# Optimization experiments

Measured on AMD Instinct MI355X. Metric: run time of the kernel, lower is better.

The kernel has to match this reference:

```python
import jax, jax.numpy as jnp
import numpy as np

N_NODES = 8192
DIM = 512

def setup_inputs() -> dict:
    key = jax.random.key(0)
    k1, k2, k3, k4 = jax.random.split(key, 4)
    x = jax.random.normal(k1, (N_NODES, DIM), dtype=jnp.float32)
    adj = jax.random.uniform(k2, (N_NODES, N_NODES), dtype=jnp.float32)
    # nn.Linear(dim, dim): weight [out, in], bias [out]
    bound = 1.0 / np.sqrt(DIM)
    W = jax.random.uniform(k3, (DIM, DIM), minval=-bound, maxval=bound, dtype=jnp.float32)
    b = jax.random.uniform(k4, (DIM,), minval=-bound, maxval=bound, dtype=jnp.float32)
    return {"x": x, "adj": adj, "W": W, "b": b}

def reference(x, adj, W, b):
    # agg = adj @ x : [N, dim]
    agg = jnp.matmul(adj, x)
    # Linear: agg @ W.T + b, then ReLU
    out = jnp.matmul(agg, W.T) + b
    return jax.nn.relu(out)
```

## Files before the change

kernel.cpp:

```cpp
#include <hip/hip_runtime.h>
#include <stdint.h>

typedef __bf16 bf16_t;
typedef bf16_t bf16x8 __attribute__((ext_vector_type(8)));
typedef float f32x4 __attribute__((ext_vector_type(4)));

#define N_NODES 8192
#define DIM 512

typedef __attribute__((address_space(1))) void as1_void;
typedef __attribute__((address_space(3))) void as3_void;

__device__ __forceinline__ void gload_lds16(const void* g, void* l) {
  __builtin_amdgcn_global_load_lds((as1_void*)g, (as3_void*)l, 16, 0, 0);
}

__global__ __launch_bounds__(256) void k_yw(const float* __restrict__ x,
                                            const float* __restrict__ W,
                                            bf16_t* __restrict__ Yt) {
  constexpr int NIT = DIM / 32;
  __shared__ float As[2][128 * 32];
  __shared__ float Bs[2][128 * 32];

  const int b = blockIdx.x;
  const int n0 = (b & 3) * 128;
  const int k0 = (b >> 2) * 128;

  const int t = threadIdx.x;
  const int lane = t & 63;
  const int w = t >> 6;
  const int wr = w & 1;
  const int wc = w >> 1;
  const int lrow = lane & 15;
  const int quad = lane >> 4;

  const int srow = t >> 3;
  const int aoff = ((t & 7) ^ (srow & 7)) * 4;
  const float* ag = W + (size_t)(n0 + srow) * DIM + aoff;
  const float* bg = x + (size_t)(k0 + srow) * DIM + aoff;

  auto stage = [&](int it, int buf) {
    const int kc = it * 32;
#pragma unroll
    for (int i = 0; i < 4; ++i) {
      gload_lds16(ag + (size_t)(i * 32) * DIM + kc, &As[buf][(i * 256 + t) * 4]);
      gload_lds16(bg + (size_t)(i * 32) * DIM + kc, &Bs[buf][(i * 256 + t) * 4]);
    }
  };

  const int apc0 = ((quad * 2) ^ (lrow & 7)) * 4;
  const int apc1 = (((quad * 2) ^ (lrow & 7)) ^ 1) * 4;

  f32x4 acc[4][4] = {};

  auto compute = [&](int buf) {
    bf16x8 af[4], bfr[4];
#pragma unroll
    for (int ii = 0; ii < 4; ++ii) {
      const int rb = (wr * 64 + ii * 16 + lrow) * 32;
      f32x4 a0 = *(const f32x4*)&As[buf][rb + apc0];
      f32x4 a1 = *(const f32x4*)&As[buf][rb + apc1];
#pragma unroll
      for (int z = 0; z < 4; ++z) {
        af[ii][z] = (bf16_t)a0[z];
        af[ii][z + 4] = (bf16_t)a1[z];
      }
    }
#pragma unroll
    for (int jj = 0; jj < 4; ++jj) {
      const int rb = (wc * 64 + jj * 16 + lrow) * 32;
      f32x4 b0 = *(const f32x4*)&Bs[buf][rb + apc0];
      f32x4 b1 = *(const f32x4*)&Bs[buf][rb + apc1];
#pragma unroll
      for (int z = 0; z < 4; ++z) {
        bfr[jj][z] = (bf16_t)b0[z];
        bfr[jj][z + 4] = (bf16_t)b1[z];
      }
    }
#pragma unroll
    for (int ii = 0; ii < 4; ++ii)
#pragma unroll
      for (int jj = 0; jj < 4; ++jj)
        acc[ii][jj] =
            __builtin_amdgcn_mfma_f32_16x16x32_bf16(af[ii], bfr[jj], acc[ii][jj], 0, 0, 0);
  };

  stage(0, 0);
  __syncthreads();
  int cur = 0;
#pragma unroll 1
  for (int it = 0; it < NIT; ++it) {
    if (it + 1 < NIT) stage(it + 1, cur ^ 1);
    compute(cur);
    __syncthreads();
    cur ^= 1;
  }

#pragma unroll
  for (int ii = 0; ii < 4; ++ii)
#pragma unroll
    for (int jj = 0; jj < 4; ++jj) {
      const int col = k0 + wc * 64 + jj * 16 + lrow;
#pragma unroll
      for (int r = 0; r < 4; ++r) {
        const int row = n0 + wr * 64 + ii * 16 + quad * 4 + r;
        Yt[(size_t)row * N_NODES + col] = (bf16_t)acc[ii][jj][r];
      }
    }
}

__global__ __launch_bounds__(256) void k_main(const float* __restrict__ A,
                                              const bf16_t* __restrict__ Bt,
                                              const float* __restrict__ bias,
                                              float* __restrict__ out) {
  constexpr int K = N_NODES;
  constexpr int NIT = K / 32;
  __shared__ float As[4][64 * 32];
  __shared__ bf16_t Bs[4][128 * 32];

  const int b = blockIdx.x;
  const int xcd = b & 7;
  const int i6 = b >> 3;
  const int n_tile = i6 & 3;
  const int mg = i6 >> 2;
  const int m0 = (mg * 8 + xcd) * 64;
  const int n0 = n_tile * 128;

  const int t = threadIdx.x;
  const int lane = t & 63;
  const int w = t >> 6;
  const int wr = w & 1;
  const int wc = w >> 1;
  const int lrow = lane & 15;
  const int quad = lane >> 4;

  const int aoff = ((t & 7) ^ ((t >> 3) & 7)) * 4;
  const int boff = ((t & 3) ^ ((t >> 3) & 3)) * 8;
  const float* ag = A + (size_t)(m0 + (t >> 3)) * K + aoff;
  const bf16_t* bg = Bt + (size_t)(n0 + (t >> 2)) * K + boff;

  auto stage = [&](int it, int buf) {
    const int kc = it * 32;
#pragma unroll
    for (int i = 0; i < 2; ++i)
      gload_lds16(ag + (size_t)(i * 32) * K + kc, &As[buf][(i * 256 + t) * 4]);
#pragma unroll
    for (int i = 0; i < 2; ++i)
      gload_lds16(bg + (size_t)(i * 64) * K + kc, &Bs[buf][(i * 256 + t) * 8]);
  };

  const int apc0 = ((quad * 2) ^ (lrow & 7)) * 4;
  const int apc1 = (((quad * 2) ^ (lrow & 7)) ^ 1) * 4;
  const int bpc = (quad ^ ((lrow >> 1) & 3)) * 8;

  f32x4 acc[2][4] = {};

  auto compute = [&](int buf) {
    bf16x8 af[2], bfr[4];
#pragma unroll
    for (int ii = 0; ii < 2; ++ii) {
      const int rb = (wr * 32 + ii * 16 + lrow) * 32;
      f32x4 a0 = *(const f32x4*)&As[buf][rb + apc0];
      f32x4 a1 = *(const f32x4*)&As[buf][rb + apc1];
#pragma unroll
      for (int z = 0; z < 4; ++z) {
        af[ii][z] = (bf16_t)a0[z];
        af[ii][z + 4] = (bf16_t)a1[z];
      }
    }
#pragma unroll
    for (int jj = 0; jj < 4; ++jj)
      bfr[jj] = *(const bf16x8*)&Bs[buf][(wc * 64 + jj * 16 + lrow) * 32 + bpc];
#pragma unroll
    for (int ii = 0; ii < 2; ++ii)
#pragma unroll
      for (int jj = 0; jj < 4; ++jj)
        acc[ii][jj] =
            __builtin_amdgcn_mfma_f32_16x16x32_bf16(af[ii], bfr[jj], acc[ii][jj], 0, 0, 0);
  };

  float bjv[4];
#pragma unroll
  for (int jj = 0; jj < 4; ++jj) bjv[jj] = bias[n0 + wc * 64 + jj * 16 + lrow];

  stage(0, 0);
  stage(1, 1);
  stage(2, 2);

#pragma unroll 1
  for (int it = 0; it < NIT; ++it) {
    if (it < NIT - 2) {
      asm volatile("s_waitcnt vmcnt(8)" ::: "memory");
    } else if (it == NIT - 2) {
      asm volatile("s_waitcnt vmcnt(4)" ::: "memory");
    } else {
      asm volatile("s_waitcnt vmcnt(0)" ::: "memory");
    }
    asm volatile("s_waitcnt lgkmcnt(0)" ::: "memory");
    asm volatile("s_barrier" ::: "memory");
    if (it + 3 < NIT) stage(it + 3, (it + 3) & 3);
    compute(it & 3);
  }

#pragma unroll
  for (int ii = 0; ii < 2; ++ii)
#pragma unroll
    for (int jj = 0; jj < 4; ++jj) {
      const int col = n0 + wc * 64 + jj * 16 + lrow;
#pragma unroll
      for (int r = 0; r < 4; ++r) {
        const int row = m0 + wr * 32 + ii * 16 + quad * 4 + r;
        float v = acc[ii][jj][r] + bjv[jj];
        out[(size_t)row * DIM + col] = v > 0.0f ? v : 0.0f;
      }
    }
}

extern "C" void kernel_launch(void* const* d_in, const int* in_sizes, int n_in,
                              void* d_out, int out_size, void* d_ws, size_t ws_size,
                              hipStream_t stream) {
  const float* x = (const float*)d_in[0];
  const float* adj = (const float*)d_in[1];
  const float* W = (const float*)d_in[2];
  const float* b = (const float*)d_in[3];
  float* out = (float*)d_out;

  bf16_t* Yt = (bf16_t*)d_ws;

  k_yw<<<dim3(256), 256, 0, stream>>>(x, W, Yt);
  k_main<<<dim3(512), 256, 0, stream>>>(adj, Yt, b, out);
}
```

Measured before the change: 581.0 us.

## Enlarge main GEMM tile to 128x128 and stream B from global into registers

Result: no change. 577.9 us (-0.5%).

```diff
diff --git a/kernel.cpp b/kernel.cpp
--- a/kernel.cpp
+++ b/kernel.cpp
@@ -115,16 +115,11 @@
                                               float* __restrict__ out) {
   constexpr int K = N_NODES;
   constexpr int NIT = K / 32;
-  __shared__ float As[4][64 * 32];
-  __shared__ bf16_t Bs[4][128 * 32];
+  __shared__ float As[4][128 * 32];
 
   const int b = blockIdx.x;
-  const int xcd = b & 7;
-  const int i6 = b >> 3;
-  const int n_tile = i6 & 3;
-  const int mg = i6 >> 2;
-  const int m0 = (mg * 8 + xcd) * 64;
-  const int n0 = n_tile * 128;
+  const int m0 = (((b >> 3) << 1) | (b & 1)) * 128;
+  const int n0 = ((b >> 1) & 3) * 128;
 
   const int t = threadIdx.x;
   const int lane = t & 63;
@@ -135,31 +130,37 @@
   const int quad = lane >> 4;
 
   const int aoff = ((t & 7) ^ ((t >> 3) & 7)) * 4;
-  const int boff = ((t & 3) ^ ((t >> 3) & 3)) * 8;
   const float* ag = A + (size_t)(m0 + (t >> 3)) * K + aoff;
-  const bf16_t* bg = Bt + (size_t)(n0 + (t >> 2)) * K + boff;
 
   auto stage = [&](int it, int buf) {
     const int kc = it * 32;
 #pragma unroll
-    for (int i = 0; i < 2; ++i)
+    for (int i = 0; i < 4; ++i)
       gload_lds16(ag + (size_t)(i * 32) * K + kc, &As[buf][(i * 256 + t) * 4]);
-#pragma unroll
-    for (int i = 0; i < 2; ++i)
-      gload_lds16(bg + (size_t)(i * 64) * K + kc, &Bs[buf][(i * 256 + t) * 8]);
   };
 
   const int apc0 = ((quad * 2) ^ (lrow & 7)) * 4;
   const int apc1 = (((quad * 2) ^ (lrow & 7)) ^ 1) * 4;
-  const int bpc = (quad ^ ((lrow >> 1) & 3)) * 8;
-
-  f32x4 acc[2][4] = {};
-
-  auto compute = [&](int buf) {
-    bf16x8 af[2], bfr[4];
-#pragma unroll
-    for (int ii = 0; ii < 2; ++ii) {
-      const int rb = (wr * 32 + ii * 16 + lrow) * 32;
+
+  const bf16_t* bsrc[4];
+#pragma unroll
+  for (int jj = 0; jj < 4; ++jj)
+    bsrc[jj] = Bt + (size_t)(n0 + wc * 64 + jj * 16 + lrow) * K + quad * 8;
+
+  bf16x8 bA[4], bB[4];
+  auto loadB = [&](int it, bf16x8* dst) {
+    const int kc = it * 32;
+#pragma unroll
+    for (int jj = 0; jj < 4; ++jj) dst[jj] = *(const bf16x8*)(bsrc[jj] + kc);
+  };
+
+  f32x4 acc[4][4] = {};
+
+  auto compute = [&](int buf, const bf16x8* bfr) {
+    bf16x8 af[4];
+#pragma unroll
+    for (int ii = 0; ii < 4; ++ii) {
+      const int rb = (wr * 64 + ii * 16 + lrow) * 32;
       f32x4 a0 = *(const f32x4*)&As[buf][rb + apc0];
       f32x4 a1 = *(const f32x4*)&As[buf][rb + apc1];
 #pragma unroll
@@ -169,48 +170,53 @@
       }
     }
 #pragma unroll
-    for (int jj = 0; jj < 4; ++jj)
-      bfr[jj] = *(const bf16x8*)&Bs[buf][(wc * 64 + jj * 16 + lrow) * 32 + bpc];
-#pragma unroll
-    for (int ii = 0; ii < 2; ++ii)
+    for (int ii = 0; ii < 4; ++ii)
 #pragma unroll
       for (int jj = 0; jj < 4; ++jj)
         acc[ii][jj] =
             __builtin_amdgcn_mfma_f32_16x16x32_bf16(af[ii], bfr[jj], acc[ii][jj], 0, 0, 0);
   };
 
-  float bjv[4];
-#pragma unroll
-  for (int jj = 0; jj < 4; ++jj) bjv[jj] = bias[n0 + wc * 64 + jj * 16 + lrow];
+  auto syncit = [&](int it) {
+    if (it < NIT - 2) {
+      asm volatile("s_waitcnt vmcnt(12)" ::: "memory");
+    } else if (it == NIT - 2) {
+      asm volatile("s_waitcnt vmcnt(8)" ::: "memory");
+    } else {
+      asm volatile("s_waitcnt vmcnt(4)" ::: "memory");
+    }
+    asm volatile("s_waitcnt lgkmcnt(0)" ::: "memory");
+    asm volatile("s_barrier" ::: "memory");
+  };
 
   stage(0, 0);
   stage(1, 1);
   stage(2, 2);
+  loadB(0, bA);
 
 #pragma unroll 1
-  for (int it = 0; it < NIT; ++it) {
-    if (it < NIT - 2) {
-      asm volatile("s_waitcnt vmcnt(8)" ::: "memory");
-    } else if (it == NIT - 2) {
-      asm volatile("s_waitcnt vmcnt(4)" ::: "memory");
-    } else {
-      asm volatile("s_waitcnt vmcnt(0)" ::: "memory");
-    }
-    asm volatile("s_waitcnt lgkmcnt(0)" ::: "memory");
-    asm volatile("s_barrier" ::: "memory");
+  for (int it = 0; it < NIT; it += 2) {
+    syncit(it);
+    loadB(it + 1, bB);
     if (it + 3 < NIT) stage(it + 3, (it + 3) & 3);
-    compute(it & 3);
+    compute(it & 3, bA);
+
+    syncit(it + 1);
+    if (it + 2 < NIT) loadB(it + 2, bA);
+    if (it + 4 < NIT) stage(it + 4, (it + 4) & 3);
+    compute((it + 1) & 3, bB);
   }
 
 #pragma unroll
-  for (int ii = 0; ii < 2; ++ii)
+  for (int ii = 0; ii < 4; ++ii)
 #pragma unroll
     for (int jj = 0; jj < 4; ++jj) {
       const int col = n0 + wc * 64 + jj * 16 + lrow;
+      const float bj = bias[col];
 #pragma unroll
       for (int r = 0; r < 4; ++r) {
-        const int row = m0 + wr * 32 + ii * 16 + quad * 4 + r;
-        float v = acc[ii][jj][r] + bjv[jj];
+        const int row = m0 + wr * 64 + ii * 16 + quad * 4 + r;
+        float v = acc[ii][jj][r] + bj;
         out[(size_t)row * DIM + col] = v > 0.0f ? v : 0.0f;
       }
     }
@@ -228,5 +234,5 @@
   bf16_t* Yt = (bf16_t*)d_ws;
 
   k_yw<<<dim3(256), 256, 0, stream>>>(x, W, Yt);
-  k_main<<<dim3(512), 256, 0, stream>>>(adj, Yt, b, out);
-}
+  k_main<<<dim3(256), 256, 0, stream>>>(adj, Yt, b, out);
+}
```

## Split-K main GEMM with larger 128x128 tiles and separate combine kernel

Applied to the files above, without the earlier changes.

New measurement: 514.8 us. 11.4% less time.

```diff
diff --git a/kernel.cpp b/kernel.cpp
--- a/kernel.cpp
+++ b/kernel.cpp
@@ -111,20 +111,18 @@
 
 __global__ __launch_bounds__(256) void k_main(const float* __restrict__ A,
                                               const bf16_t* __restrict__ Bt,
-                                              const float* __restrict__ bias,
-                                              float* __restrict__ out) {
+                                              float* __restrict__ P) {
   constexpr int K = N_NODES;
-  constexpr int NIT = K / 32;
-  __shared__ float As[4][64 * 32];
-  __shared__ bf16_t Bs[4][128 * 32];
+  constexpr int KC = 2048;
+  constexpr int NIT = KC / 32;
+  __shared__ float As[2][128 * 32];
+  __shared__ bf16_t Bs[2][128 * 32];
 
   const int b = blockIdx.x;
-  const int xcd = b & 7;
-  const int i6 = b >> 3;
-  const int n_tile = i6 & 3;
-  const int mg = i6 >> 2;
-  const int m0 = (mg * 8 + xcd) * 64;
-  const int n0 = n_tile * 128;
+  const int ks = b & 3;
+  const int n0 = ((b >> 2) & 3) * 128;
+  const int m0 = (b >> 4) * 128;
+  const int kbase = ks * KC;
 
   const int t = threadIdx.x;
   const int lane = t & 63;
@@ -136,13 +134,13 @@
 
   const int aoff = ((t & 7) ^ ((t >> 3) & 7)) * 4;
   const int boff = ((t & 3) ^ ((t >> 3) & 3)) * 8;
-  const float* ag = A + (size_t)(m0 + (t >> 3)) * K + aoff;
-  const bf16_t* bg = Bt + (size_t)(n0 + (t >> 2)) * K + boff;
+  const float* ag = A + (size_t)(m0 + (t >> 3)) * K + kbase + aoff;
+  const bf16_t* bg = Bt + (size_t)(n0 + (t >> 2)) * K + kbase + boff;
 
   auto stage = [&](int it, int buf) {
     const int kc = it * 32;
 #pragma unroll
-    for (int i = 0; i < 2; ++i)
+    for (int i = 0; i < 4; ++i)
       gload_lds16(ag + (size_t)(i * 32) * K + kc, &As[buf][(i * 256 + t) * 4]);
 #pragma unroll
     for (int i = 0; i < 2; ++i)
@@ -153,13 +151,13 @@
   const int apc1 = (((quad * 2) ^ (lrow & 7)) ^ 1) * 4;
   const int bpc = (quad ^ ((lrow >> 1) & 3)) * 8;
 
-  f32x4 acc[2][4] = {};
+  f32x4 acc[4][4] = {};
 
   auto compute = [&](int buf) {
-    bf16x8 af[2], bfr[4];
-#pragma unroll
-    for (int ii = 0; ii < 2; ++ii) {
-      const int rb = (wr * 32 + ii * 16 + lrow) * 32;
+    bf16x8 af[4], bfr[4];
+#pragma unroll
+    for (int ii = 0; ii < 4; ++ii) {
+      const int rb = (wr * 64 + ii * 16 + lrow) * 32;
       f32x4 a0 = *(const f32x4*)&As[buf][rb + apc0];
       f32x4 a1 = *(const f32x4*)&As[buf][rb + apc1];
 #pragma unroll
@@ -172,48 +170,58 @@
     for (int jj = 0; jj < 4; ++jj)
       bfr[jj] = *(const bf16x8*)&Bs[buf][(wc * 64 + jj * 16 + lrow) * 32 + bpc];
 #pragma unroll
-    for (int ii = 0; ii < 2; ++ii)
+    for (int ii = 0; ii < 4; ++ii)
 #pragma unroll
       for (int jj = 0; jj < 4; ++jj)
         acc[ii][jj] =
             __builtin_amdgcn_mfma_f32_16x16x32_bf16(af[ii], bfr[jj], acc[ii][jj], 0, 0, 0);
   };
 
-  float bjv[4];
-#pragma unroll
-  for (int jj = 0; jj < 4; ++jj) bjv[jj] = bias[n0 + wc * 64 + jj * 16 + lrow];
-
   stage(0, 0);
-  stage(1, 1);
-  stage(2, 2);
-
+  __syncthreads();
+  int cur = 0;
 #pragma unroll 1
   for (int it = 0; it < NIT; ++it) {
-    if (it < NIT - 2) {
-      asm volatile("s_waitcnt vmcnt(8)" ::: "memory");
-    } else if (it == NIT - 2) {
-      asm volatile("s_waitcnt vmcnt(4)" ::: "memory");
-    } else {
-      asm volatile("s_waitcnt vmcnt(0)" ::: "memory");
-    }
-    asm volatile("s_waitcnt lgkmcnt(0)" ::: "memory");
-    asm volatile("s_barrier" ::: "memory");
-    if (it + 3 < NIT) stage(it + 3, (it + 3) & 3);
-    compute(it & 3);
+    if (it + 1 < NIT) stage(it + 1, cur ^ 1);
+    compute(cur);
+    __syncthreads();
+    cur ^= 1;
   }
 
-#pragma unroll
-  for (int ii = 0; ii < 2; ++ii)
+  float* Pp = P + (size_t)ks * N_NODES * DIM;
+#pragma unroll
+  for (int ii = 0; ii < 4; ++ii)
 #pragma unroll
     for (int jj = 0; jj < 4; ++jj) {
       const int col = n0 + wc * 64 + jj * 16 + lrow;
 #pragma unroll
       for (int r = 0; r < 4; ++r) {
-        const int row = m0 + wr * 32 + ii * 16 + quad * 4 + r;
-        float v = acc[ii][jj][r] + bjv[jj];
-        out[(size_t)row * DIM + col] = v > 0.0f ? v : 0.0f;
-      }
-    }
+        const int row = m0 + wr * 64 + ii * 16 + quad * 4 + r;
+        Pp[(size_t)row * DIM + col] = acc[ii][jj][r];
+      }
+    }
+}
+
+__global__ __launch_bounds__(256) void k_combine(const float* __restrict__ P,
+                                                 const float* __restrict__ bias,
+                                                 float* __restrict__ out) {
+  constexpr size_t PS = (size_t)N_NODES * DIM;
+  constexpr int NV = N_NODES * DIM / 4;
+  const int stride = gridDim.x * blockDim.x;
+  for (int v = blockIdx.x * blockDim.x + threadIdx.x; v < NV; v += stride) {
+    f32x4 s0 = ((const f32x4*)P)[v];
+    f32x4 s1 = ((const f32x4*)(P + PS))[v];
+    f32x4 s2 = ((const f32x4*)(P + 2 * PS))[v];
+    f32x4 s3 = ((const f32x4*)(P + 3 * PS))[v];
+    f32x4 bv = *(const f32x4*)&bias[(v & 127) * 4];
+    f32x4 r;
+#pragma unroll
+    for (int z = 0; z < 4; ++z) {
+      float tv = s0[z] + s1[z] + s2[z] + s3[z] + bv[z];
+      r[z] = tv > 0.0f ? tv : 0.0f;
+    }
+    ((f32x4*)out)[v] = r;
+  }
 }
 
 extern "C" void kernel_launch(void* const* d_in, const int* in_sizes, int n_in,
@@ -226,7 +234,9 @@
   float* out = (float*)d_out;
 
   bf16_t* Yt = (bf16_t*)d_ws;
+  float* P = (float*)(Yt + (size_t)DIM * N_NODES);
 
   k_yw<<<dim3(256), 256, 0, stream>>>(x, W, Yt);
-  k_main<<<dim3(512), 256, 0, stream>>>(adj, Yt, b, out);
-}
+  k_main<<<dim3(1024), 256, 0, stream>>>(adj, Yt, P);
+  k_combine<<<dim3(2048), 256, 0, stream>>>(P, b, out);
+}
```
